# Performance work log

Measured on AMD Instinct MI355X. Metric: run time of the kernel, lower is better.

Reference implementation:

```python
import jax, jax.numpy as jnp
import numpy as np

B, C, P, L = 128, 5, 5, 5
D = 128
USER_NUM, TITLE_NUM, ENTITY_NUM, REL_NUM = 50000, 30000, 100000, 100


def setup_inputs() -> dict:
    key = jax.random.key(0)
    k = jax.random.split(key, 22)
    f = jnp.float32
    s = 0.1  # weight scale to keep LSTM gates in a sane range
    return {
        "candidate_newsindex": jax.random.randint(k[0], (B, C), 0, TITLE_NUM),
        "user_index": jax.random.randint(k[1], (B,), 0, USER_NUM),
        "total_paths_index": jax.random.randint(k[2], (USER_NUM, C, P, L), 0, TITLE_NUM),
        "total_type_index": jax.random.randint(k[3], (USER_NUM, C, P, L), 0, 3),
        "total_relations_index": jax.random.randint(k[4], (USER_NUM, C, P, L), 0, REL_NUM),
        "entity_emb": jax.random.normal(k[5], (ENTITY_NUM, D), f),
        "relation_emb": jax.random.normal(k[6], (REL_NUM, D), f),
        "user_emb": jax.random.normal(k[7], (USER_NUM, D), f),
        "news_emb": jax.random.normal(k[8], (TITLE_NUM, D), f),
        "type_emb": jax.random.normal(k[9], (3, D), f),
        "Wih0": jax.random.normal(k[10], (P, 4 * D, 3 * D), f) * s,
        "Whh0": jax.random.normal(k[11], (P, 4 * D, D), f) * s,
        "bih0": jax.random.normal(k[12], (P, 4 * D), f) * s,
        "bhh0": jax.random.normal(k[13], (P, 4 * D), f) * s,
        "Wih1": jax.random.normal(k[14], (P, 4 * D, D), f) * s,
        "Whh1": jax.random.normal(k[15], (P, 4 * D, D), f) * s,
        "bih1": jax.random.normal(k[16], (P, 4 * D), f) * s,
        "bhh1": jax.random.normal(k[17], (P, 4 * D), f) * s,
        "W1": jax.random.normal(k[18], (16, D), f) * s,
        "b1": jax.random.normal(k[19], (16,), f) * s,
        "W2": jax.random.normal(k[20], (1, 16), f) * s,
        "b2": jax.random.normal(k[21], (1,), f) * s,
    }


def _lstm2(x, Wih0, Whh0, bih0, bhh0, Wih1, Whh1, bih1, bhh1):
    """2-layer PyTorch-style LSTM (gate order i,f,g,o). x: [N, T, in] -> [N, T, H]."""
    def layer(x, Wih, Whh, bih, bhh):
        N = x.shape[0]
        H = Whh.shape[1]
        h0 = jnp.zeros((N, H), x.dtype)
        c0 = jnp.zeros((N, H), x.dtype)
        b = bih + bhh
        def step(carry, xt):
            h, c = carry
            g = xt @ Wih.T + h @ Whh.T + b
            i, f, gg, o = jnp.split(g, 4, axis=-1)
            c = jax.nn.sigmoid(f) * c + jax.nn.sigmoid(i) * jnp.tanh(gg)
            h = jax.nn.sigmoid(o) * jnp.tanh(c)
            return (h, c), h
        _, ys = jax.lax.scan(step, (h0, c0), x.swapaxes(0, 1))
        return ys.swapaxes(0, 1)
    x = layer(x, Wih0, Whh0, bih0, bhh0)
    x = layer(x, Wih1, Whh1, bih1, bhh1)
    return x


def reference(candidate_newsindex, user_index, total_paths_index, total_type_index,
              total_relations_index, entity_emb, relation_emb, user_emb, news_emb,
              type_emb, Wih0, Whh0, bih0, bhh0, Wih1, Whh1, bih1, bhh1,
              W1, b1, W2, b2):
    bpath = total_paths_index[user_index]  # [B,C,P,L]
    btype = total_type_index[user_index]
    brel = total_relations_index[user_index]
    # per-node embedding selected by type: 0->user, 1->news, else entity
    node = jnp.where((btype == 0)[..., None], user_emb[bpath],
                     jnp.where((btype == 1)[..., None], news_emb[bpath], entity_emb[bpath]))
    inp = jnp.concatenate([node, type_emb[btype], relation_emb[brel]], axis=-1)  # [B,C,P,L,3D]
    Bb, Cc, Pp, Ll, F = inp.shape
    x = inp.transpose(2, 0, 1, 3, 4).reshape(Pp, Bb * Cc, Ll, F)  # per-path batches
    outs = jax.vmap(_lstm2)(x, Wih0, Whh0, bih0, bhh0, Wih1, Whh1, bih1, bhh1)  # [P,BC,L,H]
    idx = jnp.arange(Pp)
    sel = outs[idx, :, idx, :]  # LSTM i's output at timestep i -> [P, BC, H]
    ps = jax.nn.sigmoid(jnp.maximum(sel @ W1.T + b1, 0.0) @ W2.T + b2)[..., 0]  # [P,BC]
    ps_mean = ps.reshape(Pp, Bb, Cc).mean(axis=0)  # [B,C]
    # faithful to source: total_output accumulates over candidates j, so the score
    # for candidate j is the cumulative mean of path scores for candidates 0..j
    total_score = jnp.cumsum(ps_mean, axis=1) / jnp.arange(1, Cc + 1, dtype=ps_mean.dtype)
    emb_score = jax.nn.sigmoid(jnp.sum(news_emb[candidate_newsindex] * user_emb[user_index][:, None, :], axis=-1))
    return emb_score + total_score
```

## Files before the change

kernel.cpp:

```cpp
#include <hip/hip_runtime.h>
#include <math.h>

#define BB   128
#define CC   5
#define PP   5
#define LL   5
#define DD   128
#define NSEQ 640
#define GATES 512
#define IN0  384
#define HPAD 136

typedef __attribute__((ext_vector_type(8))) short short8;
typedef __attribute__((ext_vector_type(4))) float f32x4;

__device__ __forceinline__ float sigf(float x){ return 1.0f/(1.0f+__expf(-x)); }
__device__ __forceinline__ float tanhfast(float x){ return 1.0f - 2.0f/(__expf(2.0f*x)+1.0f); }

__device__ __forceinline__ unsigned short f2bf(float x){
    union { float f; unsigned u; } v; v.f = x;
    unsigned r = v.u + 0x7FFF + ((v.u >> 16) & 1);
    return (unsigned short)(r >> 16);
}

__device__ __constant__ int c_ptmap[15] = {0,5,6,10,11,12,15,16,17,18,20,21,22,23,24};

__global__ void stage0_kernel(const float* __restrict__ Wih0, const float* __restrict__ Whh0,
                              const float* __restrict__ Wih1, const float* __restrict__ Whh1,
                              const float* __restrict__ bih0, const float* __restrict__ bhh0,
                              const float* __restrict__ bih1, const float* __restrict__ bhh1,
                              unsigned short* __restrict__ F0, unsigned short* __restrict__ F1,
                              unsigned short* __restrict__ F2, unsigned short* __restrict__ F3,
                              float* __restrict__ b0, float* __restrict__ b1c,
                              float* __restrict__ psum,
                              const int* __restrict__ user_index,
                              const int* __restrict__ tpath, const int* __restrict__ ttype,
                              const int* __restrict__ trel,
                              const float* __restrict__ entity_emb, const float* __restrict__ relation_emb,
                              const float* __restrict__ user_emb, const float* __restrict__ news_emb,
                              const float* __restrict__ type_emb,
                              unsigned short* __restrict__ X){
    int bx = blockIdx.x;
    if (bx < 985){
        int id = bx*256 + threadIdx.x;
        const int NF0 = PP*12*32*64;
        const int NFH = PP*4*32*64;
        if (id < NF0 + 3*NFH){
            const float* src; unsigned short* dst; int K, KT, fid;
            if (id < NF0){ src = Wih0; dst = F0; K = IN0; KT = 12; fid = id; }
            else {
                int j = id - NF0; int m = j / NFH; fid = j % NFH; K = DD; KT = 4;
                src = (m==0)?Whh0:(m==1)?Wih1:Whh1;
                dst = (m==0)?F1:(m==1)?F2:F3;
            }
            int lane = fid & 63; int rem = fid >> 6;
            int gt = rem & 31; rem >>= 5;
            int kt = rem % KT; int p = rem / KT;
            int g  = gt*16 + (lane & 15);
            int k0 = kt*32 + (lane >> 4)*8;
            const float* s = src + (size_t)(p*GATES + g)*K + k0;
            float4 x0 = *(const float4*)s;
            float4 x1 = *(const float4*)(s+4);
            uint4 o;
            o.x = f2bf(x0.x) | ((unsigned)f2bf(x0.y)<<16);
            o.y = f2bf(x0.z) | ((unsigned)f2bf(x0.w)<<16);
            o.z = f2bf(x1.x) | ((unsigned)f2bf(x1.y)<<16);
            o.w = f2bf(x1.z) | ((unsigned)f2bf(x1.w)<<16);
            *(uint4*)(dst + (size_t)fid*8) = o;
        } else {
            int j = id - (NF0 + 3*NFH);
            if (j < PP*GATES) b0[j] = bih0[j] + bhh0[j];
            else if (j < 2*PP*GATES){ int q = j - PP*GATES; b1c[q] = bih1[q] + bhh1[q]; }
            else if (j < 2*PP*GATES + NSEQ){ psum[j - 2*PP*GATES] = 0.0f; }
        }
    } else {
        int id = (bx - 985)*256 + threadIdx.x;
        if (id >= 15*NSEQ*48) return;
        int ptIdx = id / (NSEQ*48); int rem = id % (NSEQ*48);
        int n = rem / 48, q = rem % 48;
        int pt = c_ptmap[ptIdx];
        int p = pt / LL, t = pt % LL;
        int b = n / CC, c = n % CC;
        int u = user_index[b];
        int base = ((u*CC + c)*PP + p)*LL + t;
        int col = q*8;
        const float* s;
        if (q < 16){
            int ty = ttype[base]; int pi = tpath[base];
            const float* e = (ty==0)?user_emb:(ty==1)?news_emb:entity_emb;
            s = e + (size_t)pi*DD + col;
        } else if (q < 32){
            s = type_emb + (size_t)ttype[base]*DD + (col-128);
        } else {
            s = relation_emb + (size_t)trel[base]*DD + (col-256);
        }
        float4 x0 = *(const float4*)s, x1 = *(const float4*)(s+4);
        uint4 o;
        o.x = f2bf(x0.x) | ((unsigned)f2bf(x0.y)<<16);
        o.y = f2bf(x0.z) | ((unsigned)f2bf(x0.w)<<16);
        o.z = f2bf(x1.x) | ((unsigned)f2bf(x1.y)<<16);
        o.w = f2bf(x1.z) | ((unsigned)f2bf(x1.w)<<16);
        *(uint4*)(X + (size_t)(pt*NSEQ + n)*IN0 + col) = o;
    }
}

__global__ __launch_bounds__(256) void gemm_ih0_v5(const unsigned short* __restrict__ X,
                                                   const unsigned short* __restrict__ F0,
                                                   float* __restrict__ G0c){
    __shared__ unsigned short Bs[12*4*512];
    int bx = blockIdx.x;
    int nch = bx & 7;
    int m64 = (bx >> 3) % 10;
    int pt  = c_ptmap[bx / 80];
    int p = pt / LL;
    int tid = threadIdx.x, lane = tid & 63, w = tid >> 6;
    int r16 = lane & 15, qd = lane >> 4;

    const unsigned short* Fp = F0 + (((size_t)p*12)*32 + nch*4)*512;
    uint4 breg[12];
    #pragma unroll
    for (int j=0;j<12;j++)
        breg[j] = *(const uint4*)(Fp + (size_t)j*32*512 + tid*8);
    #pragma unroll
    for (int j=0;j<12;j++)
        *(uint4*)(Bs + j*2048 + tid*8) = breg[j];
    __syncthreads();

    f32x4 acc[4];
    #pragma unroll
    for (int i=0;i<4;i++) acc[i] = (f32x4)0.0f;
    const unsigned short* Xb = X + ((size_t)pt*NSEQ + m64*64 + w*16 + r16)*IN0 + qd*8;
    #pragma unroll
    for (int kt=0; kt<12; kt++){
        short8 a = *(const short8*)(Xb + kt*32);
        #pragma unroll
        for (int i=0;i<4;i++){
            short8 bfr = *(const short8*)(Bs + (kt*4+i)*512 + lane*8);
            acc[i] = __builtin_amdgcn_mfma_f32_16x16x32_bf16(a, bfr, acc[i], 0,0,0);
        }
    }
    int tile16 = pt*40 + m64*4 + w;
    float* dst = G0c + (((size_t)tile16*32 + nch*4)*64 + lane)*4;
    #pragma unroll
    for (int i=0;i<4;i++)
        *(f32x4*)(dst + (size_t)i*256) = acc[i];
}

__global__ __launch_bounds__(512, 2) void lstm_v7(
    const float* __restrict__ G0c,
    const unsigned short* __restrict__ F1,
    const unsigned short* __restrict__ F2,
    const unsigned short* __restrict__ F3,
    const float* __restrict__ b0, const float* __restrict__ b1c,
    const float* __restrict__ W1, const float* __restrict__ b1v,
    const float* __restrict__ W2, const float* __restrict__ b2v,
    float* __restrict__ psum){
    __shared__ __align__(16) unsigned short F1s[4*32*512];
    __shared__ unsigned short h0T[2][16*HPAD];
    __shared__ unsigned short h1T[2][16*HPAD];
    float* h1f  = (float*)F1s;
    float* mlpb = (float*)(F1s + 16*132*2);

    int p = blockIdx.x / 40, nt = blockIdx.x % 40;
    int n0 = nt*16;
    int tid = threadIdx.x;
    int lane = tid & 63, w = tid >> 6;
    int r16 = lane & 15, qd = lane >> 4;
    int j = w*16 + r16;

    if (p > 0){
        const unsigned short* F1g = F1 + (size_t)p*4*32*512;
        #pragma unroll 4
        for (int v=0; v<16; v++)
            *(uint4*)(F1s + v*4096 + tid*8) = *(const uint4*)(F1g + (size_t)v*4096 + tid*8);
    }

    short8 f2r[16], f3r[16];
    {
        const unsigned short* F2p = F2 + (size_t)p*4*32*512 + lane*8;
        const unsigned short* F3p = F3 + (size_t)p*4*32*512 + lane*8;
        #pragma unroll
        for (int kt=0; kt<4; kt++)
            #pragma unroll
            for (int i=0;i<4;i++){
                f2r[kt*4+i] = *(const short8*)(F2p + (size_t)(kt*32 + i*8 + w)*512);
                f3r[kt*4+i] = *(const short8*)(F3p + (size_t)(kt*32 + i*8 + w)*512);
            }
    }
    float bL0[4], bL1[4];
    #pragma unroll
    for (int i=0;i<4;i++){
        int col = (i*8 + w)*16 + r16;
        bL0[i] = b0[p*GATES + col];
        bL1[i] = b1c[p*GATES + col];
    }

    f32x4 pf[4];
    {
        const float* slab = G0c + (size_t)((p*LL + 0)*40 + nt)*8192;
        #pragma unroll
        for (int i=0;i<4;i++) pf[i] = *(const f32x4*)(slab + ((i*8+w)*64 + lane)*4);
    }
    float c0s[4] = {0,0,0,0}, c1s[4] = {0,0,0,0};

    for (int t=0; t<=p; t++){
        const int cur = t & 1, prv = cur ^ 1;
        f32x4 acc[4];
        #pragma unroll
        for (int i=0;i<4;i++){
            f32x4 a = pf[i]; float bb = bL0[i];
            a[0]+=bb; a[1]+=bb; a[2]+=bb; a[3]+=bb; acc[i]=a;
        }
        if (t < p){
            const float* ns = G0c + (size_t)((p*LL + t + 1)*40 + nt)*8192;
            #pragma unroll
            for (int i=0;i<4;i++) pf[i] = *(const f32x4*)(ns + ((i*8+w)*64 + lane)*4);
        }
        if (t > 0){
            #pragma unroll
            for (int kt=0; kt<4; kt++){
                short8 a = *(const short8*)(&h0T[prv][0] + r16*HPAD + kt*32 + qd*8);
                #pragma unroll
                for (int i=0;i<4;i++){
                    short8 bfr = *(const short8*)(F1s + (size_t)(kt*32 + i*8 + w)*512 + lane*8);
                    acc[i] = __builtin_amdgcn_mfma_f32_16x16x32_bf16(a, bfr, acc[i], 0,0,0);
                }
            }
        }
        #pragma unroll
        for (int v=0; v<4; v++){
            float cc = sigf(acc[1][v])*c0s[v] + sigf(acc[0][v])*tanhfast(acc[2][v]);
            c0s[v] = cc;
            h0T[cur][(qd*4+v)*HPAD + j] = f2bf(sigf(acc[3][v])*tanhfast(cc));
        }
        __syncthreads();
        #pragma unroll
        for (int i=0;i<4;i++){
            float bb = bL1[i];
            f32x4 a; a[0]=bb; a[1]=bb; a[2]=bb; a[3]=bb; acc[i]=a;
        }
        #pragma unroll
        for (int kt=0; kt<4; kt++){
            short8 a = *(const short8*)(&h0T[cur][0] + r16*HPAD + kt*32 + qd*8);
            #pragma unroll
            for (int i=0;i<4;i++)
                acc[i] = __builtin_amdgcn_mfma_f32_16x16x32_bf16(a, f2r[kt*4+i], acc[i], 0,0,0);
        }
        if (t > 0){
            #pragma unroll
            for (int kt=0; kt<4; kt++){
                short8 a = *(const short8*)(&h1T[prv][0] + r16*HPAD + kt*32 + qd*8);
                #pragma unroll
                for (int i=0;i<4;i++)
                    acc[i] = __builtin_amdgcn_mfma_f32_16x16x32_bf16(a, f3r[kt*4+i], acc[i], 0,0,0);
            }
        }
        #pragma unroll
        for (int v=0; v<4; v++){
            float cc = sigf(acc[1][v])*c1s[v] + sigf(acc[0][v])*tanhfast(acc[2][v]);
            c1s[v] = cc;
            float hh = sigf(acc[3][v])*tanhfast(cc);
            if (t < p) h1T[cur][(qd*4+v)*HPAD + j] = f2bf(hh);
            else       h1f[(qd*4+v)*132 + j] = hh;
        }
    }
    __syncthreads();
    if (tid < 256){
        int rr = tid & 15, hc = tid >> 4;
        const float4* w1r = (const float4*)(W1 + hc*DD);
        const float4* hrow = (const float4*)(h1f + rr*132);
        float a0 = b1v[hc], a1 = 0.0f, a2 = 0.0f, a3 = 0.0f;
        #pragma unroll
        for (int k=0;k<32;k++){
            float4 wv = w1r[k];
            float4 hv = hrow[k];
            a0 = fmaf(hv.x, wv.x, a0);
            a1 = fmaf(hv.y, wv.y, a1);
            a2 = fmaf(hv.z, wv.z, a2);
            a3 = fmaf(hv.w, wv.w, a3);
        }
        mlpb[hc*17 + rr] = fmaxf((a0+a1)+(a2+a3), 0.0f);
    }
    __syncthreads();
    if (tid < 16){
        float s = b2v[0];
        #pragma unroll
        for (int h=0;h<16;h++) s = fmaf(mlpb[h*17 + tid], W2[h], s);
        atomicAdd(&psum[n0 + tid], 0.2f*sigf(s));
    }
}

__global__ void final_kernel(const int* __restrict__ cand, const int* __restrict__ user_index,
                             const float* __restrict__ news_emb, const float* __restrict__ user_emb,
                             const float* __restrict__ psum, float* __restrict__ out){
    int b = blockIdx.x;
    int lane = threadIdx.x;
    int u = user_index[b];
    const float* ue = user_emb + (size_t)u*DD;
    float cum = 0.0f;
    for (int c=0;c<CC;c++){
        int nb = cand[b*CC + c];
        const float* ne = news_emb + (size_t)nb*DD;
        float v = ne[lane]*ue[lane] + ne[lane+64]*ue[lane+64];
        #pragma unroll
        for (int off=32; off; off>>=1) v += __shfl_down(v, off, 64);
        if (lane == 0){
            cum += psum[b*CC + c];
            out[b*CC + c] = sigf(v) + cum/(float)(c+1);
        }
    }
}

extern "C" void kernel_launch(void* const* d_in, const int* in_sizes, int n_in,
                              void* d_out, int out_size, void* d_ws, size_t ws_size,
                              hipStream_t stream){
    const int* cand        = (const int*)d_in[0];
    const int* uidx        = (const int*)d_in[1];
    const int* tpath       = (const int*)d_in[2];
    const int* ttype       = (const int*)d_in[3];
    const int* trel        = (const int*)d_in[4];
    const float* entity_emb   = (const float*)d_in[5];
    const float* relation_emb = (const float*)d_in[6];
    const float* user_emb     = (const float*)d_in[7];
    const float* news_emb     = (const float*)d_in[8];
    const float* type_emb     = (const float*)d_in[9];
    const float* Wih0 = (const float*)d_in[10];
    const float* Whh0 = (const float*)d_in[11];
    const float* bih0 = (const float*)d_in[12];
    const float* bhh0 = (const float*)d_in[13];
    const float* Wih1 = (const float*)d_in[14];
    const float* Whh1 = (const float*)d_in[15];
    const float* bih1 = (const float*)d_in[16];
    const float* bhh1 = (const float*)d_in[17];
    const float* W1 = (const float*)d_in[18];
    const float* b1 = (const float*)d_in[19];
    const float* W2 = (const float*)d_in[20];
    const float* b2 = (const float*)d_in[21];
    float* out = (float*)d_out;

    char* ws = (char*)d_ws;
    unsigned short* F0 = (unsigned short*)ws;  ws += (size_t)PP*12*32*512*2;
    unsigned short* F1 = (unsigned short*)ws;  ws += (size_t)PP*4*32*512*2;
    unsigned short* F2 = (unsigned short*)ws;  ws += (size_t)PP*4*32*512*2;
    unsigned short* F3 = (unsigned short*)ws;  ws += (size_t)PP*4*32*512*2;
    float* b0  = (float*)ws;                   ws += PP*GATES*4;
    float* b1c = (float*)ws;                   ws += PP*GATES*4;
    unsigned short* X = (unsigned short*)ws;   ws += (size_t)PP*LL*NSEQ*IN0*2;
    float* G0c = (float*)ws;                   ws += (size_t)PP*LL*NSEQ*GATES*4;
    float* psum = (float*)ws;                  ws += NSEQ*4;

    stage0_kernel<<<985+1800,256,0,stream>>>(Wih0,Whh0,Wih1,Whh1,bih0,bhh0,bih1,bhh1,
                                             F0,F1,F2,F3,b0,b1c,psum,
                                             uidx,tpath,ttype,trel,entity_emb,relation_emb,
                                             user_emb,news_emb,type_emb,X);
    gemm_ih0_v5<<<1200,256,0,stream>>>(X, F0, G0c);
    lstm_v7<<<200,512,0,stream>>>(G0c, F1, F2, F3, b0, b1c, W1, b1, W2, b2, psum);
    final_kernel<<<BB,64,0,stream>>>(cand, uidx, news_emb, user_emb, psum, out);
}
```

Measured before the change: 225.1 us.

## Fold final kernel into LSTM via last-block counter and async LDS weight load

Removes the separate final kernel launch. The user/candidate embedding dot products now run as extra blocks in stage0, and the last LSTM block to finish (found with an atomic counter) computes the cumulative scores and writes the output. The F1 weight copy into shared memory also switches to global_load_lds direct-to-LDS loads, so the data no longer passes through registers. This saves one launch and its gap, at the cost of an extra threadfence and atomic in every LSTM block.

```diff
diff --git a/kernel.cpp b/kernel.cpp
--- a/kernel.cpp
+++ b/kernel.cpp
@@ -13,6 +13,8 @@
 
 typedef __attribute__((ext_vector_type(8))) short short8;
 typedef __attribute__((ext_vector_type(4))) float f32x4;
+typedef __attribute__((address_space(1))) const unsigned int as1_uint;
+typedef __attribute__((address_space(3))) unsigned int as3_uint;
 
 __device__ __forceinline__ float sigf(float x){ return 1.0f/(1.0f+__expf(-x)); }
 __device__ __forceinline__ float tanhfast(float x){ return 1.0f - 2.0f/(__expf(2.0f*x)+1.0f); }
@@ -39,7 +41,9 @@
                               const float* __restrict__ entity_emb, const float* __restrict__ relation_emb,
                               const float* __restrict__ user_emb, const float* __restrict__ news_emb,
                               const float* __restrict__ type_emb,
-                              unsigned short* __restrict__ X){
+                              unsigned short* __restrict__ X,
+                              const int* __restrict__ cand,
+                              float* __restrict__ embv, int* __restrict__ ctr){
     int bx = blockIdx.x;
     if (bx < 985){
         int id = bx*256 + threadIdx.x;
@@ -72,8 +76,9 @@
             if (j < PP*GATES) b0[j] = bih0[j] + bhh0[j];
             else if (j < 2*PP*GATES){ int q = j - PP*GATES; b1c[q] = bih1[q] + bhh1[q]; }
             else if (j < 2*PP*GATES + NSEQ){ psum[j - 2*PP*GATES] = 0.0f; }
-        }
-    } else {
+            else if (j == 2*PP*GATES + NSEQ){ ctr[0] = 0; }
+        }
+    } else if (bx < 2785){
         int id = (bx - 985)*256 + threadIdx.x;
         if (id >= 15*NSEQ*48) return;
         int ptIdx = id / (NSEQ*48); int rem = id % (NSEQ*48);
@@ -101,6 +106,20 @@
         o.z = f2bf(x1.x) | ((unsigned)f2bf(x1.y)<<16);
         o.w = f2bf(x1.z) | ((unsigned)f2bf(x1.w)<<16);
         *(uint4*)(X + (size_t)(pt*NSEQ + n)*IN0 + col) = o;
+    } else {
+        int id = (bx - 2785)*256 + threadIdx.x;
+        int n = id >> 4, k = id & 15;
+        int b = n / CC;
+        int nb = cand[n];
+        int u = user_index[b];
+        const float4* ne = (const float4*)(news_emb + (size_t)nb*DD + k*8);
+        const float4* ue = (const float4*)(user_emb + (size_t)u*DD + k*8);
+        float4 a0 = ne[0], a1 = ne[1], u0 = ue[0], u1 = ue[1];
+        float v = a0.x*u0.x + a0.y*u0.y + a0.z*u0.z + a0.w*u0.w
+                + a1.x*u1.x + a1.y*u1.y + a1.z*u1.z + a1.w*u1.w;
+        #pragma unroll
+        for (int off=8; off; off>>=1) v += __shfl_down(v, off, 16);
+        if (k == 0) embv[n] = v;
     }
 }
 
@@ -146,7 +165,7 @@
         *(f32x4*)(dst + (size_t)i*256) = acc[i];
 }
 
-__global__ __launch_bounds__(512, 2) void lstm_v7(
+__global__ __launch_bounds__(512, 2) void lstm_v8(
     const float* __restrict__ G0c,
     const unsigned short* __restrict__ F1,
     const unsigned short* __restrict__ F2,
@@ -154,10 +173,13 @@
     const float* __restrict__ b0, const float* __restrict__ b1c,
     const float* __restrict__ W1, const float* __restrict__ b1v,
     const float* __restrict__ W2, const float* __restrict__ b2v,
-    float* __restrict__ psum){
+    float* __restrict__ psum,
+    const float* __restrict__ embv, int* __restrict__ ctr,
+    float* __restrict__ out){
     __shared__ __align__(16) unsigned short F1s[4*32*512];
     __shared__ unsigned short h0T[2][16*HPAD];
     __shared__ unsigned short h1T[2][16*HPAD];
+    __shared__ int lastFlag;
     float* h1f  = (float*)F1s;
     float* mlpb = (float*)(F1s + 16*132*2);
 
@@ -170,9 +192,13 @@
 
     if (p > 0){
         const unsigned short* F1g = F1 + (size_t)p*4*32*512;
-        #pragma unroll 4
-        for (int v=0; v<16; v++)
-            *(uint4*)(F1s + v*4096 + tid*8) = *(const uint4*)(F1g + (size_t)v*4096 + tid*8);
+        #pragma unroll
+        for (int v=0; v<16; v++){
+            __builtin_amdgcn_global_load_lds(
+                (as1_uint*)(F1g + (size_t)v*4096 + tid*8),
+                (as3_uint*)(F1s + v*4096 + (tid & 448)*8),
+                16, 0, 0);
+        }
     }
 
     short8 f2r[16], f3r[16];
@@ -287,26 +313,25 @@
         #pragma unroll
         for (int h=0;h<16;h++) s = fmaf(mlpb[h*17 + tid], W2[h], s);
         atomicAdd(&psum[n0 + tid], 0.2f*sigf(s));
-    }
-}
-
-__global__ void final_kernel(const int* __restrict__ cand, const int* __restrict__ user_index,
-                             const float* __restrict__ news_emb, const float* __restrict__ user_emb,
-                             const float* __restrict__ psum, float* __restrict__ out){
-    int b = blockIdx.x;
-    int lane = threadIdx.x;
-    int u = user_index[b];
-    const float* ue = user_emb + (size_t)u*DD;
-    float cum = 0.0f;
-    for (int c=0;c<CC;c++){
-        int nb = cand[b*CC + c];
-        const float* ne = news_emb + (size_t)nb*DD;
-        float v = ne[lane]*ue[lane] + ne[lane+64]*ue[lane+64];
-        #pragma unroll
-        for (int off=32; off; off>>=1) v += __shfl_down(v, off, 64);
-        if (lane == 0){
-            cum += psum[b*CC + c];
-            out[b*CC + c] = sigf(v) + cum/(float)(c+1);
+        __threadfence();
+    }
+    __syncthreads();
+    if (tid == 0){
+        int old = atomicAdd(ctr, 1);
+        lastFlag = (old == 199);
+    }
+    __syncthreads();
+    if (!lastFlag) return;
+    float* ps = (float*)F1s;
+    for (int i = tid; i < NSEQ; i += 512)
+        ps[i] = atomicAdd(&psum[i], 0.0f);
+    __syncthreads();
+    if (tid < BB){
+        float cum = 0.0f;
+        #pragma unroll
+        for (int c=0;c<CC;c++){
+            cum += ps[tid*CC + c];
+            out[tid*CC + c] = sigf(embv[tid*CC + c]) + cum/(float)(c+1);
         }
     }
 }
@@ -348,12 +373,15 @@
     unsigned short* X = (unsigned short*)ws;   ws += (size_t)PP*LL*NSEQ*IN0*2;
     float* G0c = (float*)ws;                   ws += (size_t)PP*LL*NSEQ*GATES*4;
     float* psum = (float*)ws;                  ws += NSEQ*4;
-
-    stage0_kernel<<<985+1800,256,0,stream>>>(Wih0,Whh0,Wih1,Whh1,bih0,bhh0,bih1,bhh1,
+    float* embv = (float*)ws;                  ws += NSEQ*4;
+    int*   ctr  = (int*)ws;                    ws += 4;
+
+    stage0_kernel<<<985+1800+40,256,0,stream>>>(Wih0,Whh0,Wih1,Whh1,bih0,bhh0,bih1,bhh1,
                                              F0,F1,F2,F3,b0,b1c,psum,
                                              uidx,tpath,ttype,trel,entity_emb,relation_emb,
-                                             user_emb,news_emb,type_emb,X);
+                                             user_emb,news_emb,type_emb,X,
+                                             cand,embv,ctr);
     gemm_ih0_v5<<<1200,256,0,stream>>>(X, F0, G0c);
-    lstm_v7<<<200,512,0,stream>>>(G0c, F1, F2, F3, b0, b1c, W1, b1, W2, b2, psum);
-    final_kernel<<<BB,64,0,stream>>>(cand, uidx, news_emb, user_emb, psum, out);
-}
+    lstm_v8<<<200,512,0,stream>>>(G0c, F1, F2, F3, b0, b1c, W1, b1, W2, b2,
+                                  psum, embv, ctr, out);
+}
```

Measured after the change: 221.4 us. About the same (-1.6%).
